# Performance work log

Measured on AMD Instinct MI355X. Metric: run time of the kernel, lower is better.

## Reference

```python
import jax, jax.numpy as jnp
import numpy as np

N = 50000      # nodes per node type
E = 800000     # edges per meta-step (avg degree 16)
DIN = 16       # input feature dim (all node types)
DMSG = 16      # dim_message per meta-step
F = 16         # edge feature dim
DOUT = 32      # dim_out of final linear


def setup_inputs() -> dict:
    key = jax.random.key(0)
    ks = jax.random.split(key, 17)
    s = 0.1  # param scale
    return {
        "x_indivi": jax.random.normal(ks[0], (N, DIN), jnp.float32),
        "x_src_a": jax.random.normal(ks[1], (N, DIN), jnp.float32),
        "x_src_b": jax.random.normal(ks[2], (N, DIN), jnp.float32),
        "edge_index_a": jax.random.randint(ks[3], (2, E), 0, N),
        "edge_index_b": jax.random.randint(ks[4], (2, E), 0, N),
        "edge_attr_a": jax.random.normal(ks[5], (E, F), jnp.float32),
        "edge_attr_b": jax.random.normal(ks[6], (E, F), jnp.float32),
        # message_function of NNConv: Linear(F, DIN*DMSG), stored as [F, DIN, DMSG]
        "w_msg_a": jax.random.normal(ks[7], (F, DIN, DMSG), jnp.float32) * s,
        "b_msg_a": jax.random.normal(ks[8], (DIN, DMSG), jnp.float32) * s,
        "root_a": jax.random.normal(ks[9], (DIN, DMSG), jnp.float32) * s,
        "bias_a": jax.random.normal(ks[10], (DMSG,), jnp.float32) * s,
        "w_msg_b": jax.random.normal(ks[11], (F, DIN, DMSG), jnp.float32) * s,
        "b_msg_b": jax.random.normal(ks[12], (DIN, DMSG), jnp.float32) * s,
        "root_b": jax.random.normal(ks[13], (DIN, DMSG), jnp.float32) * s,
        "bias_b": jax.random.normal(ks[14], (DMSG,), jnp.float32) * s,
        # final linear: Linear(2*DMSG, DOUT), stored as [2*DMSG, DOUT]
        "w_lin": jax.random.normal(ks[15], (2 * DMSG, DOUT), jnp.float32) * s,
        "b_lin": jax.random.normal(ks[16], (DOUT,), jnp.float32) * s,
    }


def _nnconv(x_src, x_dst, edge_index, edge_attr, w_msg, b_msg, root, bias):
    """PyG NNConv with sum aggregation.
    W_e = edge_attr @ w_msg + b_msg  (per-edge [DIN, DMSG] weight matrix)
    msg_e = x_src[src_e] @ W_e ; out = segment_sum(msg) + x_dst @ root + bias
    """
    src, dst = edge_index[0], edge_index[1]
    xj = x_src[src]  # [E, DIN] gather
    # fused per-edge bmm: einsum contracts without keeping W_e longer than needed
    msg = jnp.einsum('ef,fio,ei->eo', edge_attr, w_msg, xj) + xj @ b_msg  # [E, DMSG]
    agg = jax.ops.segment_sum(msg, dst, num_segments=x_dst.shape[0])  # scatter-add
    return agg + x_dst @ root + bias


def reference(x_indivi, x_src_a, x_src_b, edge_index_a, edge_index_b,
              edge_attr_a, edge_attr_b,
              w_msg_a, b_msg_a, root_a, bias_a,
              w_msg_b, b_msg_b, root_b, bias_b,
              w_lin, b_lin):
    msg_a = jax.nn.sigmoid(_nnconv(x_src_a, x_indivi, edge_index_a, edge_attr_a,
                                   w_msg_a, b_msg_a, root_a, bias_a))
    msg_b = jax.nn.sigmoid(_nnconv(x_src_b, x_indivi, edge_index_b, edge_attr_b,
                                   w_msg_b, b_msg_b, root_b, bias_b))
    msg_cat = jnp.concatenate([msg_a, msg_b], axis=1)  # [N, 2*DMSG]
    return jax.nn.sigmoid(msg_cat @ w_lin + b_lin)     # [N, DOUT]
```

## Files before the change

kernel.cpp:

```cpp
#include <hip/hip_runtime.h>
#include <stdint.h>


#define NN 50000
#define EE 800000
#define YROW 272

__device__ __forceinline__ float bf2f(unsigned short u) {
    union { unsigned int i; float f; } v; v.i = ((unsigned int)u) << 16; return v.f;
}
__device__ __forceinline__ unsigned short f2bf(float f) {
    union { float fl; unsigned int i; } v; v.fl = f;
    unsigned int x = v.i;
    x += 0x7FFFu + ((x >> 16) & 1u);
    return (unsigned short)(x >> 16);
}

__global__ __launch_bounds__(256) void build_y(
    const float* __restrict__ x, const float* __restrict__ w_msg,
    const float* __restrict__ b_msg, unsigned short* __restrict__ y)
{
    __shared__ float sw[17 * 256];
    int tid = threadIdx.x;
    for (int idx = tid; idx < 17 * 256; idx += 256)
        sw[idx] = (idx < 4096) ? w_msg[idx] : b_msg[idx - 4096];
    __syncthreads();

    int n = blockIdx.x * 16 + (tid >> 4);
    if (n >= NN) return;
    int o = tid & 15;
    int lane = tid & 63;
    int gb = lane & ~15;

    float xv = x[n * 16 + o];
    float xi[16];
    #pragma unroll
    for (int i = 0; i < 16; ++i) xi[i] = __shfl(xv, gb + i);

    #pragma unroll
    for (int f = 0; f < 17; ++f) {
        float acc = 0.f;
        #pragma unroll
        for (int i = 0; i < 16; ++i)
            acc += xi[i] * sw[f * 256 + i * 16 + o];
        y[(size_t)n * YROW + f * 16 + o] = f2bf(acc);
    }
}

__global__ __launch_bounds__(256) void edge_msg(
    const int* __restrict__ eidx, const float* __restrict__ attr,
    const unsigned short* __restrict__ y, float* __restrict__ agg)
{
    int tid = threadIdx.x;
    int e = blockIdx.x * 16 + (tid >> 4);
    if (e >= EE) return;
    int o = tid & 15;
    int lane = tid & 63;
    int gb = lane & ~15;

    int src = eidx[e];
    int dst = eidx[EE + e];
    float av = attr[e * 16 + o];
    const unsigned short* yr = y + (size_t)src * YROW;

    float acc = bf2f(yr[256 + o]);
    #pragma unroll
    for (int f = 0; f < 16; ++f) {
        float af = __shfl(av, gb + f);
        acc += af * bf2f(yr[f * 16 + o]);
    }
    atomicAdd(&agg[(size_t)dst * 16 + o], acc);
}

__global__ __launch_bounds__(256) void finalize(
    const float* __restrict__ xind,
    const float* __restrict__ agg_a, const float* __restrict__ agg_b,
    const float* __restrict__ root_a, const float* __restrict__ bias_a,
    const float* __restrict__ root_b, const float* __restrict__ bias_b,
    const float* __restrict__ w_lin, const float* __restrict__ b_lin,
    float* __restrict__ out)
{
    int tid = threadIdx.x;
    int n = blockIdx.x * 8 + (tid >> 5);
    if (n >= NN) return;
    int d = tid & 31;
    int lane = tid & 63;
    int gb32 = lane & ~31;

    float xv = xind[n * 16 + (d & 15)];

    int j = d & 15;
    const float* root = (d < 16) ? root_a : root_b;
    const float* bias = (d < 16) ? bias_a : bias_b;
    const float* agg  = (d < 16) ? agg_a  : agg_b;

    float acc = agg[n * 16 + j] + bias[j];
    #pragma unroll
    for (int i = 0; i < 16; ++i) {
        float xiv = __shfl(xv, gb32 + i);
        acc += xiv * root[i * 16 + j];
    }
    float h = 1.f / (1.f + __expf(-acc));

    float acc2 = b_lin[d];
    #pragma unroll
    for (int jj = 0; jj < 32; ++jj) {
        float hj = __shfl(h, gb32 + jj);
        acc2 += hj * w_lin[jj * 32 + d];
    }
    out[(size_t)n * 32 + d] = 1.f / (1.f + __expf(-acc2));
}

extern "C" void kernel_launch(void* const* d_in, const int* in_sizes, int n_in,
                              void* d_out, int out_size, void* d_ws, size_t ws_size,
                              hipStream_t stream) {
    (void)in_sizes; (void)n_in; (void)out_size; (void)ws_size;
    const float* x_indivi = (const float*)d_in[0];
    const float* x_src_a  = (const float*)d_in[1];
    const float* x_src_b  = (const float*)d_in[2];
    const int*   ei_a     = (const int*)d_in[3];
    const int*   ei_b     = (const int*)d_in[4];
    const float* ea_a     = (const float*)d_in[5];
    const float* ea_b     = (const float*)d_in[6];
    const float* w_msg_a  = (const float*)d_in[7];
    const float* b_msg_a  = (const float*)d_in[8];
    const float* root_a   = (const float*)d_in[9];
    const float* bias_a   = (const float*)d_in[10];
    const float* w_msg_b  = (const float*)d_in[11];
    const float* b_msg_b  = (const float*)d_in[12];
    const float* root_b   = (const float*)d_in[13];
    const float* bias_b   = (const float*)d_in[14];
    const float* w_lin    = (const float*)d_in[15];
    const float* b_lin    = (const float*)d_in[16];
    float* out = (float*)d_out;

    char* ws = (char*)d_ws;
    size_t off = 0;
    unsigned short* y_a = (unsigned short*)(ws + off); off += (size_t)NN * YROW * 2;
    unsigned short* y_b = (unsigned short*)(ws + off); off += (size_t)NN * YROW * 2;
    float* agg_a = (float*)(ws + off); off += (size_t)NN * 16 * 4;
    float* agg_b = (float*)(ws + off); off += (size_t)NN * 16 * 4;

    hipMemsetAsync(agg_a, 0, (size_t)NN * 16 * 4 * 2, stream);

    build_y<<<(NN + 15) / 16, 256, 0, stream>>>(x_src_a, w_msg_a, b_msg_a, y_a);
    build_y<<<(NN + 15) / 16, 256, 0, stream>>>(x_src_b, w_msg_b, b_msg_b, y_b);

    edge_msg<<<(EE + 15) / 16, 256, 0, stream>>>(ei_a, ea_a, y_a, agg_a);
    edge_msg<<<(EE + 15) / 16, 256, 0, stream>>>(ei_b, ea_b, y_b, agg_b);

    finalize<<<(NN + 7) / 8, 256, 0, stream>>>(
        x_indivi, agg_a, agg_b, root_a, bias_a, root_b, bias_b, w_lin, b_lin, out);
}
```

Measured before the change: 341.1 us.

## Vectorize edge gather with 8 lanes per edge and reuse one Y buffer

The edge kernel now assigns 8 threads per edge, loading the 544-byte bf16 Y row with 16-byte vector loads and the edge attributes via shared memory. Partial products are combined across lanes with xor shuffles before the atomic adds, so each thread issues two atomics instead of one per output. The launch order is also changed so a single Y workspace is built and consumed per edge type, shrinking the workspace and its cache footprint. This aims to cut the many small scalar gathers, at the cost of extra shuffle reductions and a block barrier.

```diff
diff --git a/kernel.cpp b/kernel.cpp
--- a/kernel.cpp
+++ b/kernel.cpp
@@ -14,6 +14,12 @@
     unsigned int x = v.i;
     x += 0x7FFFu + ((x >> 16) & 1u);
     return (unsigned short)(x >> 16);
+}
+__device__ __forceinline__ float blo(unsigned int d) {
+    union { unsigned int u; float f; } v; v.u = d << 16; return v.f;
+}
+__device__ __forceinline__ float bhi(unsigned int d) {
+    union { unsigned int u; float f; } v; v.u = d & 0xFFFF0000u; return v.f;
 }
 
 __global__ __launch_bounds__(256) void build_y(
@@ -51,25 +57,64 @@
     const int* __restrict__ eidx, const float* __restrict__ attr,
     const unsigned short* __restrict__ y, float* __restrict__ agg)
 {
+    __shared__ float abuf[32][18];
     int tid = threadIdx.x;
-    int e = blockIdx.x * 16 + (tid >> 4);
-    if (e >= EE) return;
-    int o = tid & 15;
-    int lane = tid & 63;
-    int gb = lane & ~15;
+    int slot = tid >> 3;
+    int l = tid & 7;
+    int e = blockIdx.x * 32 + slot;
+    int h = l & 1, q = l >> 1;
 
     int src = eidx[e];
     int dst = eidx[EE + e];
-    float av = attr[e * 16 + o];
-    const unsigned short* yr = y + (size_t)src * YROW;
 
-    float acc = bf2f(yr[256 + o]);
+    const uint4* row = (const uint4*)(y + (size_t)src * YROW);
+    uint4 v0 = row[l];
+    uint4 v1 = row[8 + l];
+    uint4 v2 = row[16 + l];
+    uint4 v3 = row[24 + l];
+    uint4 vb = row[32 + h];
+    float2 av = ((const float2*)(attr + (size_t)e * 16))[l];
+    ((float2*)&abuf[slot][0])[l] = av;
+    __syncthreads();
+
+    float p[8];
+    if (q == 0) {
+        p[0] = blo(vb.x); p[1] = bhi(vb.x); p[2] = blo(vb.y); p[3] = bhi(vb.y);
+        p[4] = blo(vb.z); p[5] = bhi(vb.z); p[6] = blo(vb.w); p[7] = bhi(vb.w);
+    } else {
+        #pragma unroll
+        for (int j = 0; j < 8; ++j) p[j] = 0.f;
+    }
+
+    float a0 = abuf[slot][q];
+    float a1 = abuf[slot][4 + q];
+    float a2 = abuf[slot][8 + q];
+    float a3 = abuf[slot][12 + q];
+
+    p[0] += a0 * blo(v0.x); p[1] += a0 * bhi(v0.x); p[2] += a0 * blo(v0.y); p[3] += a0 * bhi(v0.y);
+    p[4] += a0 * blo(v0.z); p[5] += a0 * bhi(v0.z); p[6] += a0 * blo(v0.w); p[7] += a0 * bhi(v0.w);
+    p[0] += a1 * blo(v1.x); p[1] += a1 * bhi(v1.x); p[2] += a1 * blo(v1.y); p[3] += a1 * bhi(v1.y);
+    p[4] += a1 * blo(v1.z); p[5] += a1 * bhi(v1.z); p[6] += a1 * blo(v1.w); p[7] += a1 * bhi(v1.w);
+    p[0] += a2 * blo(v2.x); p[1] += a2 * bhi(v2.x); p[2] += a2 * blo(v2.y); p[3] += a2 * bhi(v2.y);
+    p[4] += a2 * blo(v2.z); p[5] += a2 * bhi(v2.z); p[6] += a2 * blo(v2.w); p[7] += a2 * bhi(v2.w);
+    p[0] += a3 * blo(v3.x); p[1] += a3 * bhi(v3.x); p[2] += a3 * blo(v3.y); p[3] += a3 * bhi(v3.y);
+    p[4] += a3 * blo(v3.z); p[5] += a3 * bhi(v3.z); p[6] += a3 * blo(v3.w); p[7] += a3 * bhi(v3.w);
+
     #pragma unroll
-    for (int f = 0; f < 16; ++f) {
-        float af = __shfl(av, gb + f);
-        acc += af * bf2f(yr[f * 16 + o]);
-    }
-    atomicAdd(&agg[(size_t)dst * 16 + o], acc);
+    for (int j = 0; j < 8; ++j) p[j] += __shfl_xor(p[j], 2);
+    #pragma unroll
+    for (int j = 0; j < 8; ++j) p[j] += __shfl_xor(p[j], 4);
+
+    float t0 = (q & 1) ? p[1] : p[0];
+    float t1 = (q & 1) ? p[3] : p[2];
+    float w1 = (q & 2) ? t1 : t0;
+    float s0 = (q & 1) ? p[5] : p[4];
+    float s1 = (q & 1) ? p[7] : p[6];
+    float w2 = (q & 2) ? s1 : s0;
+
+    int ob = dst * 16 + 8 * h + q;
+    atomicAdd(&agg[ob], w1);
+    atomicAdd(&agg[ob + 4], w2);
 }
 
 __global__ __launch_bounds__(256) void finalize(
@@ -136,18 +181,17 @@
 
     char* ws = (char*)d_ws;
     size_t off = 0;
-    unsigned short* y_a = (unsigned short*)(ws + off); off += (size_t)NN * YROW * 2;
-    unsigned short* y_b = (unsigned short*)(ws + off); off += (size_t)NN * YROW * 2;
+    unsigned short* ybuf = (unsigned short*)(ws + off); off += (size_t)NN * YROW * 2;
     float* agg_a = (float*)(ws + off); off += (size_t)NN * 16 * 4;
     float* agg_b = (float*)(ws + off); off += (size_t)NN * 16 * 4;
 
     hipMemsetAsync(agg_a, 0, (size_t)NN * 16 * 4 * 2, stream);
 
-    build_y<<<(NN + 15) / 16, 256, 0, stream>>>(x_src_a, w_msg_a, b_msg_a, y_a);
-    build_y<<<(NN + 15) / 16, 256, 0, stream>>>(x_src_b, w_msg_b, b_msg_b, y_b);
+    build_y<<<(NN + 15) / 16, 256, 0, stream>>>(x_src_a, w_msg_a, b_msg_a, ybuf);
+    edge_msg<<<EE / 32, 256, 0, stream>>>(ei_a, ea_a, ybuf, agg_a);
 
-    edge_msg<<<(EE + 15) / 16, 256, 0, stream>>>(ei_a, ea_a, y_a, agg_a);
-    edge_msg<<<(EE + 15) / 16, 256, 0, stream>>>(ei_b, ea_b, y_b, agg_b);
+    build_y<<<(NN + 15) / 16, 256, 0, stream>>>(x_src_b, w_msg_b, b_msg_b, ybuf);
+    edge_msg<<<EE / 32, 256, 0, stream>>>(ei_b, ea_b, ybuf, agg_b);
 
     finalize<<<(NN + 7) / 8, 256, 0, stream>>>(
         x_indivi, agg_a, agg_b, root_a, bias_a, root_b, bias_b, w_lin, b_lin, out);
```

Result: slower. 378.4 us (+10.9%).

## Replace per-node Y precompute with per-edge MFMA over outer-product features

Applied to the files above, without the earlier changes.

Drops the build_y pass, which materialised a 272-wide bf16 row per source node, along with the per-edge gather of that row. Instead each wave processes 16 edges: it forms the bf16 outer product of edge_attr and x_src[src] as the A operand and multiplies it by the prepacked w_msg/b_msg fragments held in registers using mfma_f32_16x16x32_bf16. The edge kernel becomes a persistent grid-stride loop over 1024 blocks. This removes a large intermediate write and read, at the cost of extra packing ALU work, a small weight-prep kernel, and bf16 rounding of the attr*x products.

```diff
diff --git a/kernel.cpp b/kernel.cpp
--- a/kernel.cpp
+++ b/kernel.cpp
@@ -1,75 +1,97 @@
 #include <hip/hip_runtime.h>
+#include <hip/hip_bf16.h>
 #include <stdint.h>
 
 
 #define NN 50000
 #define EE 800000
-#define YROW 272
 
-__device__ __forceinline__ float bf2f(unsigned short u) {
-    union { unsigned int i; float f; } v; v.i = ((unsigned int)u) << 16; return v.f;
-}
-__device__ __forceinline__ unsigned short f2bf(float f) {
+typedef __attribute__((ext_vector_type(8))) short short8;
+typedef __attribute__((ext_vector_type(4))) float f32x4;
+
+union U8 { short8 v; unsigned int u[4]; };
+
+__device__ __forceinline__ unsigned short f2bf_rne(float f) {
     union { float fl; unsigned int i; } v; v.fl = f;
     unsigned int x = v.i;
     x += 0x7FFFu + ((x >> 16) & 1u);
     return (unsigned short)(x >> 16);
 }
 
-__global__ __launch_bounds__(256) void build_y(
-    const float* __restrict__ x, const float* __restrict__ w_msg,
-    const float* __restrict__ b_msg, unsigned short* __restrict__ y)
-{
-    __shared__ float sw[17 * 256];
-    int tid = threadIdx.x;
-    for (int idx = tid; idx < 17 * 256; idx += 256)
-        sw[idx] = (idx < 4096) ? w_msg[idx] : b_msg[idx - 4096];
-    __syncthreads();
+__device__ __forceinline__ unsigned int pack2bf(float a, float b) {
+    __hip_bfloat162 h = __float22bfloat162_rn(float2{a, b});
+    union { __hip_bfloat162 h2; unsigned int u; } c; c.h2 = h;
+    return c.u;
+}
 
-    int n = blockIdx.x * 16 + (tid >> 4);
-    if (n >= NN) return;
-    int o = tid & 15;
-    int lane = tid & 63;
-    int gb = lane & ~15;
-
-    float xv = x[n * 16 + o];
-    float xi[16];
-    #pragma unroll
-    for (int i = 0; i < 16; ++i) xi[i] = __shfl(xv, gb + i);
-
-    #pragma unroll
-    for (int f = 0; f < 17; ++f) {
-        float acc = 0.f;
-        #pragma unroll
-        for (int i = 0; i < 16; ++i)
-            acc += xi[i] * sw[f * 256 + i * 16 + o];
-        y[(size_t)n * YROW + f * 16 + o] = f2bf(acc);
+__global__ void prep_w(const float* __restrict__ w_msg, const float* __restrict__ b_msg,
+                       unsigned short* __restrict__ wfrag) {
+    for (int idx = threadIdx.x; idx < 9 * 64 * 8; idx += 256) {
+        int j = idx & 7;
+        int lane = (idx >> 3) & 63;
+        int t = idx >> 9;
+        int k = 32 * t + (lane >> 4) * 8 + j;
+        int n = lane & 15;
+        int f = k >> 4, i = k & 15;
+        float v = (f < 16) ? w_msg[f * 256 + i * 16 + n]
+                           : (f == 16 ? b_msg[i * 16 + n] : 0.f);
+        wfrag[idx] = f2bf_rne(v);
     }
 }
 
-__global__ __launch_bounds__(256) void edge_msg(
+__global__ __launch_bounds__(256) void edge_mfma(
     const int* __restrict__ eidx, const float* __restrict__ attr,
-    const unsigned short* __restrict__ y, float* __restrict__ agg)
+    const float* __restrict__ x, const unsigned short* __restrict__ wfrag,
+    float* __restrict__ agg)
 {
-    int tid = threadIdx.x;
-    int e = blockIdx.x * 16 + (tid >> 4);
-    if (e >= EE) return;
-    int o = tid & 15;
-    int lane = tid & 63;
-    int gb = lane & ~15;
+    int lane = threadIdx.x & 63;
+    int m = lane & 15, quad = lane >> 4;
+    int q2 = quad >> 1, qb = quad & 1;
+    int wave = (blockIdx.x * 256 + (int)threadIdx.x) >> 6;
+    int nwaves = (gridDim.x * 256) >> 6;
 
-    int src = eidx[e];
-    int dst = eidx[EE + e];
-    float av = attr[e * 16 + o];
-    const unsigned short* yr = y + (size_t)src * YROW;
+    short8 bfr[9];
+    #pragma unroll
+    for (int t = 0; t < 9; ++t)
+        bfr[t] = ((const short8*)wfrag)[t * 64 + lane];
 
-    float acc = bf2f(yr[256 + o]);
-    #pragma unroll
-    for (int f = 0; f < 16; ++f) {
-        float af = __shfl(av, gb + f);
-        acc += af * bf2f(yr[f * 16 + o]);
+    for (int g = wave; g < EE / 16; g += nwaves) {
+        int ebase = g * 16;
+        int src = eidx[ebase + m];
+        int dstr[4];
+        #pragma unroll
+        for (int r = 0; r < 4; ++r)
+            dstr[r] = eidx[EE + ebase + quad * 4 + r];
+
+        const float4* xr = (const float4*)(x + (size_t)src * 16);
+        float4 x0 = xr[qb * 2];
+        float4 x1 = xr[qb * 2 + 1];
+        float xh[8] = {x0.x, x0.y, x0.z, x0.w, x1.x, x1.y, x1.z, x1.w};
+
+        const float* ar = attr + (size_t)(ebase + m) * 16;
+        float ah[8];
+        #pragma unroll
+        for (int t = 0; t < 8; ++t) ah[t] = ar[2 * t + q2];
+
+        f32x4 acc = {0.f, 0.f, 0.f, 0.f};
+        #pragma unroll
+        for (int t = 0; t < 8; ++t) {
+            U8 a;
+            #pragma unroll
+            for (int jj = 0; jj < 4; ++jj)
+                a.u[jj] = pack2bf(ah[t] * xh[2 * jj], ah[t] * xh[2 * jj + 1]);
+            acc = __builtin_amdgcn_mfma_f32_16x16x32_bf16(a.v, bfr[t], acc, 0, 0, 0);
+        }
+        U8 a8;
+        #pragma unroll
+        for (int jj = 0; jj < 4; ++jj)
+            a8.u[jj] = (q2 == 0) ? pack2bf(xh[2 * jj], xh[2 * jj + 1]) : 0u;
+        acc = __builtin_amdgcn_mfma_f32_16x16x32_bf16(a8.v, bfr[8], acc, 0, 0, 0);
+
+        #pragma unroll
+        for (int r = 0; r < 4; ++r)
+            atomicAdd(&agg[dstr[r] * 16 + m], acc[r]);
     }
-    atomicAdd(&agg[(size_t)dst * 16 + o], acc);
 }
 
 __global__ __launch_bounds__(256) void finalize(
@@ -136,18 +158,17 @@
 
     char* ws = (char*)d_ws;
     size_t off = 0;
-    unsigned short* y_a = (unsigned short*)(ws + off); off += (size_t)NN * YROW * 2;
-    unsigned short* y_b = (unsigned short*)(ws + off); off += (size_t)NN * YROW * 2;
+    unsigned short* wf_a = (unsigned short*)(ws + off); off += 9 * 64 * 8 * 2;
+    unsigned short* wf_b = (unsigned short*)(ws + off); off += 9 * 64 * 8 * 2;
     float* agg_a = (float*)(ws + off); off += (size_t)NN * 16 * 4;
     float* agg_b = (float*)(ws + off); off += (size_t)NN * 16 * 4;
 
     hipMemsetAsync(agg_a, 0, (size_t)NN * 16 * 4 * 2, stream);
+    prep_w<<<1, 256, 0, stream>>>(w_msg_a, b_msg_a, wf_a);
+    prep_w<<<1, 256, 0, stream>>>(w_msg_b, b_msg_b, wf_b);
 
-    build_y<<<(NN + 15) / 16, 256, 0, stream>>>(x_src_a, w_msg_a, b_msg_a, y_a);
-    build_y<<<(NN + 15) / 16, 256, 0, stream>>>(x_src_b, w_msg_b, b_msg_b, y_b);
-
-    edge_msg<<<(EE + 15) / 16, 256, 0, stream>>>(ei_a, ea_a, y_a, agg_a);
-    edge_msg<<<(EE + 15) / 16, 256, 0, stream>>>(ei_b, ea_b, y_b, agg_b);
+    edge_mfma<<<1024, 256, 0, stream>>>(ei_a, ea_a, x_src_a, wf_a, agg_a);
+    edge_mfma<<<1024, 256, 0, stream>>>(ei_b, ea_b, x_src_b, wf_b, agg_b);
 
     finalize<<<(NN + 7) / 8, 256, 0, stream>>>(
         x_indivi, agg_a, agg_b, root_a, bias_a, root_b, bias_b, w_lin, b_lin, out);
```

Result: faster. 304.3 us (-10.8%).
